# Kernel tuning notes

Hardware: AMD Instinct MI355X
Metric: run time of the kernel (lower is better)

Reference implementation:

```python
import jax, jax.numpy as jnp
import numpy as np

T = 0.5  # sharpening temperature
M, N, DK, DV = 8192, 8192, 512, 512


def setup_inputs() -> dict:
    key = jax.random.key(0)
    kq, kk, kv = jax.random.split(key, 3)
    Q = jax.random.normal(kq, (M, DK), dtype=jnp.float32)
    K = jax.random.normal(kk, (N, DK), dtype=jnp.float32)
    V = jax.random.normal(kv, (N, DV), dtype=jnp.float32)
    return {"Q": Q, "K": K, "V": V}


def reference(Q, K, V):
    d_k = K.shape[1]
    scores = jnp.matmul(Q, K.T) / np.sqrt(d_k)          # (m, n)
    attn = jax.nn.softmax(scores, axis=-1)              # (m, n)
    # sharpen: p^(1/T), renormalize over keys (dim=1 for 2D == last axis)
    u = jnp.power(attn, 1.0 / T)
    attn = u / jnp.sum(u, axis=1, keepdims=True)
    return jnp.matmul(attn, V)                          # (m, d_v)
```

## Files before the change

kernel.cpp:

```cpp
#include <hip/hip_runtime.h>

typedef unsigned short u16;
typedef __attribute__((ext_vector_type(8))) short bf16x8;
typedef __attribute__((ext_vector_type(4))) float f32x4;
typedef __attribute__((ext_vector_type(4))) u16 u16x4;

#define MFMA16(a, b, c) __builtin_amdgcn_mfma_f32_16x16x32_bf16(a, b, c, 0, 0, 0)

__device__ __forceinline__ u16 f2bf(float f) {
    union { float f; unsigned u; } v; v.f = f;
    unsigned r = (v.u + 0x7FFFu + ((v.u >> 16) & 1u)) >> 16;
    return (u16)r;
}

__device__ __forceinline__ void gload_lds16(const void* g, void* l) {
    __builtin_amdgcn_global_load_lds((const __attribute__((address_space(1))) void*)g,
                                     (__attribute__((address_space(3))) void*)l, 16, 0, 0);
}

__global__ __launch_bounds__(256) void cvt_kernel(const float* __restrict__ src,
                                                  u16* __restrict__ dst, int n4, float scale) {
    int i = blockIdx.x * 256 + threadIdx.x;
    if (i >= n4) return;
    f32x4 v = *(const f32x4*)(src + (size_t)i * 4);
    u16x4 o;
#pragma unroll
    for (int j = 0; j < 4; ++j) o[j] = f2bf(v[j] * scale);
    *(u16x4*)(dst + (size_t)i * 4) = o;
}

__global__ __launch_bounds__(256) void prep_vt(const float* __restrict__ V, u16* __restrict__ Vt) {
    __shared__ float tile[64][65];
    int t = threadIdx.x;
    int n0 = blockIdx.x * 64;
    int d0 = blockIdx.y * 64;
    int tr = t >> 4, tc = t & 15;
#pragma unroll
    for (int p = 0; p < 4; ++p) {
        int n = p * 16 + tr;
        f32x4 v = *(const f32x4*)(V + (size_t)(n0 + n) * 512 + d0 + tc * 4);
#pragma unroll
        for (int j = 0; j < 4; ++j) tile[n][tc * 4 + j] = v[j];
    }
    __syncthreads();
#pragma unroll
    for (int p = 0; p < 4; ++p) {
        int d = p * 16 + tr;
        u16x4 o;
#pragma unroll
        for (int j = 0; j < 4; ++j) o[j] = f2bf(tile[tc * 4 + j][d]);
        *(u16x4*)(Vt + (size_t)(d0 + d) * 8192 + n0 + tc * 4) = o;
    }
}

__global__ __launch_bounds__(512) void flash_kernel(
    const u16* __restrict__ Qs, const u16* __restrict__ Kb, const u16* __restrict__ Vt,
    float* __restrict__ Opart, float* __restrict__ lpart) {
    __shared__ __align__(16) u16 lds_k[128 * 512];
    __shared__ __align__(16) u16 lds_p[64 * 128];
    __shared__ float s_l[2][64];

    const int tid = threadIdx.x;
    const int wid = tid >> 6;
    const int lane = tid & 63;
    const int lo = lane & 15;
    const int hi = lane >> 4;
    const int mi = wid >> 1;
    const int nj = wid & 1;

    const int bx = blockIdx.x;
    const int x = bx & 7;
    const int g = bx >> 3;
    const int ks = x >> 2;
    const int mtile = g * 4 + (x & 3);
    const int key0 = ks * 4096;

    bf16x8 qf[16];
    {
        const u16* qrow = Qs + (size_t)(mtile * 64 + mi * 16 + lo) * 512 + hi * 8;
#pragma unroll
        for (int kt = 0; kt < 16; ++kt) qf[kt] = *(const bf16x8*)(qrow + kt * 32);
    }

    f32x4 o[4][4];
#pragma unroll
    for (int a = 0; a < 4; ++a)
#pragma unroll
        for (int b = 0; b < 4; ++b) o[a][b] = (f32x4){0.f, 0.f, 0.f, 0.f};
    float lsum = 0.f;
    bf16x8 vbA[4][2], vbB[4][2];

    const int cbase = ((hi ^ (lo & 3)) + ((lo >> 2) & 1) * 4) * 8;
    const int rowA_A = (nj * 32 + lo) * 512;
    const int rowA_B = rowA_A + 64 * 512;

    const int qrow = mi * 16 + lo;
    const int chA0 = ((nj * 4 + (hi >> 1)) ^ (qrow & 7));
    const int chA1 = ((nj * 4 + 2 + (hi >> 1)) ^ (qrow & 7));
    const int pwA0 = qrow * 128 + (chA0 << 3) + (hi & 1) * 4;
    const int pwA1 = qrow * 128 + (chA1 << 3) + (hi & 1) * 4;
    const int pwB0 = pwA0 + 64;
    const int pwB1 = pwA1 + 64;

#define STAGE_K(IT)                                                                 \
    {                                                                               \
        const u16* kb_ = Kb + (size_t)(key0 + (IT) * 128) * 512;                    \
        _Pragma("unroll") for (int r_ = 0; r_ < 16; ++r_) {                         \
            int row_ = (wid << 4) + r_;                                             \
            gload_lds16(kb_ + (size_t)row_ * 512 + ((lane ^ (row_ & 7)) << 3),      \
                        &lds_k[row_ * 512]);                                        \
        }                                                                           \
    }

#define S_COMPUTE(ROWBASE, S0A, S0B, S1A, S1B)                                      \
    {                                                                               \
        const u16* pAe = &lds_k[0] + (ROWBASE) + cbase;                             \
        const u16* pAo = &lds_k[0] + (ROWBASE) + (cbase ^ 32);                      \
        const u16* pBe = pAe + 16 * 512;                                            \
        const u16* pBo = pAo + 16 * 512;                                            \
        _Pragma("unroll") for (int kt2 = 0; kt2 < 8; ++kt2) {                       \
            bf16x8 ae = *(const bf16x8*)(pAe + kt2 * 64);                           \
            bf16x8 be = *(const bf16x8*)(pBe + kt2 * 64);                           \
            bf16x8 ao = *(const bf16x8*)(pAo + kt2 * 64);                           \
            bf16x8 bo = *(const bf16x8*)(pBo + kt2 * 64);                           \
            S0A = MFMA16(ae, qf[2 * kt2], S0A);                                     \
            S1A = MFMA16(be, qf[2 * kt2], S1A);                                     \
            S0B = MFMA16(ao, qf[2 * kt2 + 1], S0B);                                 \
            S1B = MFMA16(bo, qf[2 * kt2 + 1], S1B);                                 \
        }                                                                           \
    }

#define PV_STEP(CH_OFF, VB)                                                         \
    {                                                                               \
        _Pragma("unroll") for (int mt = 0; mt < 4; ++mt) {                          \
            int m = mt * 16 + lo;                                                   \
            int c0 = (CH_OFF) + (hi ^ (m & 7));                                     \
            int c1 = (CH_OFF) + ((4 + hi) ^ (m & 7));                               \
            bf16x8 pa0 = *(const bf16x8*)(&lds_p[m * 128 + c0 * 8]);                \
            bf16x8 pa1 = *(const bf16x8*)(&lds_p[m * 128 + c1 * 8]);                \
            _Pragma("unroll") for (int nt = 0; nt < 4; ++nt) {                      \
                f32x4 c_ = o[mt][nt];                                               \
                c_ = MFMA16(pa0, VB[nt][0], c_);                                    \
                c_ = MFMA16(pa1, VB[nt][1], c_);                                    \
                o[mt][nt] = c_;                                                     \
            }                                                                       \
        }                                                                           \
    }

#define EXP_PW(S0, S1, PW0, PW1)                                                    \
    {                                                                               \
        u16x4 w0, w1;                                                               \
        _Pragma("unroll") for (int r = 0; r < 4; ++r) {                             \
            float p0 = __expf((S0)[r]);                                             \
            float p1 = __expf((S1)[r]);                                             \
            lsum += p0 + p1;                                                        \
            w0[r] = f2bf(p0);                                                       \
            w1[r] = f2bf(p1);                                                       \
        }                                                                           \
        *(u16x4*)(&lds_p[PW0]) = w0;                                                \
        *(u16x4*)(&lds_p[PW1]) = w1;                                                \
    }

#define VB_LOAD(T, KOFF, VB)                                                        \
    {                                                                               \
        _Pragma("unroll") for (int nt = 0; nt < 4; ++nt) {                          \
            const u16* vrow = Vt + (size_t)(wid * 64 + nt * 16 + lo) * 8192 +       \
                              key0 + (T) * 128 + (KOFF) + hi * 8;                   \
            VB[nt][0] = *(const bf16x8*)(vrow);                                     \
            VB[nt][1] = *(const bf16x8*)(vrow + 32);                                \
        }                                                                           \
    }

    STAGE_K(0)
    asm volatile("s_waitcnt vmcnt(0)\n\ts_barrier" ::: "memory");

    for (int t = 0; t < 32; ++t) {
        VB_LOAD(t, 0, vbA)
        f32x4 a0a = {0.f, 0.f, 0.f, 0.f}, a0b = a0a, a1a = a0a, a1b = a0a;
        __builtin_amdgcn_s_setprio(1);
        S_COMPUTE(rowA_A, a0a, a0b, a1a, a1b)
        __builtin_amdgcn_s_setprio(0);
        f32x4 sA0 = a0a + a0b, sA1 = a1a + a1b;
        EXP_PW(sA0, sA1, pwA0, pwA1)

        VB_LOAD(t, 64, vbB)
        f32x4 b0a = {0.f, 0.f, 0.f, 0.f}, b0b = b0a, b1a = b0a, b1b = b0a;
        __builtin_amdgcn_s_setprio(1);
        S_COMPUTE(rowA_B, b0a, b0b, b1a, b1b)
        __builtin_amdgcn_s_setprio(0);
        f32x4 sB0 = b0a + b0b, sB1 = b1a + b1b;
        EXP_PW(sB0, sB1, pwB0, pwB1)

        asm volatile("s_waitcnt lgkmcnt(0)\n\ts_barrier" ::: "memory");

        if (t < 31) STAGE_K(t + 1)

        __builtin_amdgcn_s_setprio(1);
        PV_STEP(0, vbA)
        PV_STEP(8, vbB)
        __builtin_amdgcn_s_setprio(0);

        if (t < 31) asm volatile("s_waitcnt vmcnt(0) lgkmcnt(0)\n\ts_barrier" ::: "memory");
    }

    lsum += __shfl_xor(lsum, 16);
    lsum += __shfl_xor(lsum, 32);
    if (lane < 16) s_l[nj][qrow] = lsum;
    __syncthreads();

    const int lb = mtile * 2 + ks;
    {
        float* Ob = Opart + (size_t)lb * (64 * 512);
#pragma unroll
        for (int mt = 0; mt < 4; ++mt)
#pragma unroll
            for (int nt = 0; nt < 4; ++nt)
#pragma unroll
                for (int r = 0; r < 4; ++r) {
                    int row = mt * 16 + hi * 4 + r;
                    int col = wid * 64 + nt * 16 + lo;
                    Ob[row * 512 + col] = o[mt][nt][r];
                }
        if (tid < 64) {
            lpart[lb * 64 + tid] = s_l[0][tid] + s_l[1][tid];
        }
    }
}

__global__ __launch_bounds__(256) void combine_kernel(const float* __restrict__ Opart,
                                                      const float* __restrict__ lpart,
                                                      float* __restrict__ out) {
    int i = blockIdx.x * 256 + threadIdx.x;
    int row = i >> 7;
    int c4 = i & 127;
    int mtile = row >> 6, rl = row & 63;
    int b0 = mtile * 2, b1 = b0 + 1;
    float inv = 1.0f / (lpart[b0 * 64 + rl] + lpart[b1 * 64 + rl]);
    f32x4 a = *(const f32x4*)(Opart + (size_t)b0 * 32768 + rl * 512 + c4 * 4);
    f32x4 b = *(const f32x4*)(Opart + (size_t)b1 * 32768 + rl * 512 + c4 * 4);
    f32x4 r = (a + b) * inv;
    *(f32x4*)(out + (size_t)row * 512 + c4 * 4) = r;
}

extern "C" void kernel_launch(void* const* d_in, const int* in_sizes, int n_in,
                              void* d_out, int out_size, void* d_ws, size_t ws_size,
                              hipStream_t stream) {
    const float* Q = (const float*)d_in[0];
    const float* K = (const float*)d_in[1];
    const float* V = (const float*)d_in[2];
    float* out = (float*)d_out;
    char* ws = (char*)d_ws;

    u16* Qs = (u16*)(ws + 0);
    u16* Kb = (u16*)(ws + 8388608);
    u16* Vt = (u16*)(ws + 16777216);
    float* Op = (float*)(ws + 25165824);
    float* lp = (float*)(ws + 58720256);

    const float scale = 0.08838834764831845f;
    cvt_kernel<<<4096, 256, 0, stream>>>(Q, Qs, 1048576, scale);
    cvt_kernel<<<4096, 256, 0, stream>>>(K, Kb, 1048576, 1.0f);
    prep_vt<<<dim3(128, 8), 256, 0, stream>>>(V, Vt);
    flash_kernel<<<256, 512, 0, stream>>>(Qs, Kb, Vt, Op, lp);
    combine_kernel<<<4096, 256, 0, stream>>>(Op, lp, out);
}
```

Before: 215.5 us.

## Remap S-tile wave layout so each K fragment feeds two query row tiles

Waves now own 32 query rows by 16 keys instead of 16 rows by 32 keys. Each loaded K fragment is reused across two Q row tiles held in registers, which halves the LDS reads of K per MFMA at the cost of doubling the Q fragment registers. The softmax exponent switches to exp2f, with log2(e) folded into the Q prescale. V fragment loads move after the barrier into scoped blocks, which shortens their register lifetime but exposes V load latency right before the PV MFMAs.

After: 304.6 us. 41.4% more time.

```diff
diff --git a/kernel.cpp b/kernel.cpp
--- a/kernel.cpp
+++ b/kernel.cpp
@@ -58,15 +58,15 @@
     float* __restrict__ Opart, float* __restrict__ lpart) {
     __shared__ __align__(16) u16 lds_k[128 * 512];
     __shared__ __align__(16) u16 lds_p[64 * 128];
-    __shared__ float s_l[2][64];
+    __shared__ float s_l[4][64];
 
     const int tid = threadIdx.x;
     const int wid = tid >> 6;
     const int lane = tid & 63;
     const int lo = lane & 15;
     const int hi = lane >> 4;
-    const int mi = wid >> 1;
-    const int nj = wid & 1;
+    const int ks4 = wid & 3;
+    const int rs = wid >> 2;
 
     const int bx = blockIdx.x;
     const int x = bx & 7;
@@ -75,11 +75,12 @@
     const int mtile = g * 4 + (x & 3);
     const int key0 = ks * 4096;
 
-    bf16x8 qf[16];
-    {
-        const u16* qrow = Qs + (size_t)(mtile * 64 + mi * 16 + lo) * 512 + hi * 8;
-#pragma unroll
-        for (int kt = 0; kt < 16; ++kt) qf[kt] = *(const bf16x8*)(qrow + kt * 32);
+    bf16x8 qf[2][16];
+#pragma unroll
+    for (int rt = 0; rt < 2; ++rt) {
+        const u16* qrow = Qs + (size_t)(mtile * 64 + rs * 32 + rt * 16 + lo) * 512 + hi * 8;
+#pragma unroll
+        for (int kt = 0; kt < 16; ++kt) qf[rt][kt] = *(const bf16x8*)(qrow + kt * 32);
     }
 
     f32x4 o[4][4];
@@ -87,20 +88,14 @@
     for (int a = 0; a < 4; ++a)
 #pragma unroll
         for (int b = 0; b < 4; ++b) o[a][b] = (f32x4){0.f, 0.f, 0.f, 0.f};
-    float lsum = 0.f;
-    bf16x8 vbA[4][2], vbB[4][2];
+    float lsum0 = 0.f, lsum1 = 0.f;
 
     const int cbase = ((hi ^ (lo & 3)) + ((lo >> 2) & 1) * 4) * 8;
-    const int rowA_A = (nj * 32 + lo) * 512;
+    const int rowA_A = (ks4 * 16 + lo) * 512;
     const int rowA_B = rowA_A + 64 * 512;
 
-    const int qrow = mi * 16 + lo;
-    const int chA0 = ((nj * 4 + (hi >> 1)) ^ (qrow & 7));
-    const int chA1 = ((nj * 4 + 2 + (hi >> 1)) ^ (qrow & 7));
-    const int pwA0 = qrow * 128 + (chA0 << 3) + (hi & 1) * 4;
-    const int pwA1 = qrow * 128 + (chA1 << 3) + (hi & 1) * 4;
-    const int pwB0 = pwA0 + 64;
-    const int pwB1 = pwA1 + 64;
+    const int row0 = rs * 32 + lo;
+    const int pwA = row0 * 128 + ((((ks4 << 1) + (hi >> 1)) ^ (row0 & 7)) << 3) + (hi & 1) * 4;
 
 #define STAGE_K(IT)                                                                 \
     {                                                                               \
@@ -112,22 +107,33 @@
         }                                                                           \
     }
 
-#define S_COMPUTE(ROWBASE, S0A, S0B, S1A, S1B)                                      \
+#define S_COMPUTE(ROWBASE, SE0, SO0, SE1, SO1)                                      \
     {                                                                               \
         const u16* pAe = &lds_k[0] + (ROWBASE) + cbase;                             \
         const u16* pAo = &lds_k[0] + (ROWBASE) + (cbase ^ 32);                      \
-        const u16* pBe = pAe + 16 * 512;                                            \
-        const u16* pBo = pAo + 16 * 512;                                            \
         _Pragma("unroll") for (int kt2 = 0; kt2 < 8; ++kt2) {                       \
             bf16x8 ae = *(const bf16x8*)(pAe + kt2 * 64);                           \
-            bf16x8 be = *(const bf16x8*)(pBe + kt2 * 64);                           \
             bf16x8 ao = *(const bf16x8*)(pAo + kt2 * 64);                           \
-            bf16x8 bo = *(const bf16x8*)(pBo + kt2 * 64);                           \
-            S0A = MFMA16(ae, qf[2 * kt2], S0A);                                     \
-            S1A = MFMA16(be, qf[2 * kt2], S1A);                                     \
-            S0B = MFMA16(ao, qf[2 * kt2 + 1], S0B);                                 \
-            S1B = MFMA16(bo, qf[2 * kt2 + 1], S1B);                                 \
-        }                                                                           \
+            SE0 = MFMA16(ae, qf[0][2 * kt2], SE0);                                  \
+            SE1 = MFMA16(ae, qf[1][2 * kt2], SE1);                                  \
+            SO0 = MFMA16(ao, qf[0][2 * kt2 + 1], SO0);                              \
+            SO1 = MFMA16(ao, qf[1][2 * kt2 + 1], SO1);                              \
+        }                                                                           \
+    }
+
+#define EXP_PW(SRT0, SRT1, BOFS)                                                    \
+    {                                                                               \
+        u16x4 w0, w1;                                                               \
+        _Pragma("unroll") for (int r = 0; r < 4; ++r) {                             \
+            float p0 = exp2f((SRT0)[r]);                                            \
+            float p1 = exp2f((SRT1)[r]);                                            \
+            lsum0 += p0;                                                            \
+            lsum1 += p1;                                                            \
+            w0[r] = f2bf(p0);                                                       \
+            w1[r] = f2bf(p1);                                                       \
+        }                                                                           \
+        *(u16x4*)(&lds_p[pwA + (BOFS)]) = w0;                                       \
+        *(u16x4*)(&lds_p[pwA + 2048 + (BOFS)]) = w1;                                \
     }
 
 #define PV_STEP(CH_OFF, VB)                                                         \
@@ -147,20 +153,6 @@
         }                                                                           \
     }
 
-#define EXP_PW(S0, S1, PW0, PW1)                                                    \
-    {                                                                               \
-        u16x4 w0, w1;                                                               \
-        _Pragma("unroll") for (int r = 0; r < 4; ++r) {                             \
-            float p0 = __expf((S0)[r]);                                             \
-            float p1 = __expf((S1)[r]);                                             \
-            lsum += p0 + p1;                                                        \
-            w0[r] = f2bf(p0);                                                       \
-            w1[r] = f2bf(p1);                                                       \
-        }                                                                           \
-        *(u16x4*)(&lds_p[PW0]) = w0;                                                \
-        *(u16x4*)(&lds_p[PW1]) = w1;                                                \
-    }
-
 #define VB_LOAD(T, KOFF, VB)                                                        \
     {                                                                               \
         _Pragma("unroll") for (int nt = 0; nt < 4; ++nt) {                          \
@@ -175,37 +167,50 @@
     asm volatile("s_waitcnt vmcnt(0)\n\ts_barrier" ::: "memory");
 
     for (int t = 0; t < 32; ++t) {
-        VB_LOAD(t, 0, vbA)
-        f32x4 a0a = {0.f, 0.f, 0.f, 0.f}, a0b = a0a, a1a = a0a, a1b = a0a;
+        f32x4 ae0 = {0.f, 0.f, 0.f, 0.f}, ao0 = ae0, ae1 = ae0, ao1 = ae0;
         __builtin_amdgcn_s_setprio(1);
-        S_COMPUTE(rowA_A, a0a, a0b, a1a, a1b)
+        S_COMPUTE(rowA_A, ae0, ao0, ae1, ao1)
         __builtin_amdgcn_s_setprio(0);
-        f32x4 sA0 = a0a + a0b, sA1 = a1a + a1b;
-        EXP_PW(sA0, sA1, pwA0, pwA1)
-
-        VB_LOAD(t, 64, vbB)
-        f32x4 b0a = {0.f, 0.f, 0.f, 0.f}, b0b = b0a, b1a = b0a, b1b = b0a;
+        f32x4 sA0 = ae0 + ao0, sA1 = ae1 + ao1;
+        EXP_PW(sA0, sA1, 0)
+
+        f32x4 be0 = {0.f, 0.f, 0.f, 0.f}, bo0 = be0, be1 = be0, bo1 = be0;
         __builtin_amdgcn_s_setprio(1);
-        S_COMPUTE(rowA_B, b0a, b0b, b1a, b1b)
+        S_COMPUTE(rowA_B, be0, bo0, be1, bo1)
         __builtin_amdgcn_s_setprio(0);
-        f32x4 sB0 = b0a + b0b, sB1 = b1a + b1b;
-        EXP_PW(sB0, sB1, pwB0, pwB1)
+        f32x4 sB0 = be0 + bo0, sB1 = be1 + bo1;
+        EXP_PW(sB0, sB1, 64)
 
         asm volatile("s_waitcnt lgkmcnt(0)\n\ts_barrier" ::: "memory");
 
         if (t < 31) STAGE_K(t + 1)
 
-        __builtin_amdgcn_s_setprio(1);
-        PV_STEP(0, vbA)
-        PV_STEP(8, vbB)
-        __builtin_amdgcn_s_setprio(0);
+        {
+            bf16x8 vbA[4][2];
+            VB_LOAD(t, 0, vbA)
+            __builtin_amdgcn_s_setprio(1);
+            PV_STEP(0, vbA)
+            __builtin_amdgcn_s_setprio(0);
+        }
+        {
+            bf16x8 vbB[4][2];
+            VB_LOAD(t, 64, vbB)
+            __builtin_amdgcn_s_setprio(1);
+            PV_STEP(8, vbB)
+            __builtin_amdgcn_s_setprio(0);
+        }
 
         if (t < 31) asm volatile("s_waitcnt vmcnt(0) lgkmcnt(0)\n\ts_barrier" ::: "memory");
     }
 
-    lsum += __shfl_xor(lsum, 16);
-    lsum += __shfl_xor(lsum, 32);
-    if (lane < 16) s_l[nj][qrow] = lsum;
+    lsum0 += __shfl_xor(lsum0, 16);
+    lsum0 += __shfl_xor(lsum0, 32);
+    lsum1 += __shfl_xor(lsum1, 16);
+    lsum1 += __shfl_xor(lsum1, 32);
+    if (lane < 16) {
+        s_l[ks4][rs * 32 + lo] = lsum0;
+        s_l[ks4][rs * 32 + 16 + lo] = lsum1;
+    }
     __syncthreads();
 
     const int lb = mtile * 2 + ks;
@@ -222,7 +227,7 @@
                     Ob[row * 512 + col] = o[mt][nt][r];
                 }
         if (tid < 64) {
-            lpart[lb * 64 + tid] = s_l[0][tid] + s_l[1][tid];
+            lpart[lb * 64 + tid] = s_l[0][tid] + s_l[1][tid] + s_l[2][tid] + s_l[3][tid];
         }
     }
 }
@@ -257,7 +262,7 @@
     float* Op = (float*)(ws + 25165824);
     float* lp = (float*)(ws + 58720256);
 
-    const float scale = 0.08838834764831845f;
+    const float scale = 0.12751743576842596f;
     cvt_kernel<<<4096, 256, 0, stream>>>(Q, Qs, 1048576, scale);
     cvt_kernel<<<4096, 256, 0, stream>>>(K, Kb, 1048576, 1.0f);
     prep_vt<<<dim3(128, 8), 256, 0, stream>>>(V, Vt);
```
